# Optimization experiments

Hardware: AMD Instinct MI355X
Metric: run time of the kernel (lower is better)

Reference implementation:

```python
import jax, jax.numpy as jnp
import numpy as np
from jax import lax

GROUPS = 32
EPS = 1e-5
N_STEPS = 8   # fixed-step stand-in for adaptive implicit_adams
N_CORR = 2    # trapezoidal (Adams-Moulton) corrector iterations


def group_norm(x, gamma, beta):
    B, C, H, W = x.shape
    xg = x.reshape(B, GROUPS, C // GROUPS, H, W)
    mean = xg.mean(axis=(2, 3, 4), keepdims=True)
    var = xg.var(axis=(2, 3, 4), keepdims=True)
    xg = (xg - mean) * lax.rsqrt(var + EPS)
    return xg.reshape(B, C, H, W) * gamma[None, :, None, None] + beta[None, :, None, None]


def batch_norm1d(x, gamma, beta):  # training-mode batch stats, x: [B,C,L]
    mean = x.mean(axis=(0, 2), keepdims=True)
    var = x.var(axis=(0, 2), keepdims=True)
    return (x - mean) * lax.rsqrt(var + EPS) * gamma[None, :, None] + beta[None, :, None]


def conv1d(x, w, b):  # x [B,Cin,L], w [Cout,Cin,3], pad=1
    y = lax.conv_general_dilated(x, w, (1,), [(1, 1)], dimension_numbers=('NCH', 'OIH', 'NCH'))
    return y + b[None, :, None]


def concat_conv2d(t, x, w, b):  # x [B,C,H,W], w [C, C+1, 3,3], pad=1
    tt = jnp.full_like(x[:, :1], t)
    ttx = jnp.concatenate([tt, x], axis=1)
    y = lax.conv_general_dilated(ttx, w, (1, 1), [(1, 1), (1, 1)], dimension_numbers=('NCHW', 'OIHW', 'NCHW'))
    return y + b[None, :, None, None]


def make_odefunc(cw1, cb1, gn1_g, gn1_b, gn2_g, gn2_b, cw2, cb2, gn3_g, gn3_b):
    def f(t, x):
        out = jax.nn.relu(group_norm(x, gn1_g, gn1_b))
        out = concat_conv2d(t, out, cw1, cb1)
        out = jax.nn.elu(group_norm(out, gn2_g, gn2_b))
        out = concat_conv2d(t, out, cw2, cb2)
        return group_norm(out, gn3_g, gn3_b)
    return f


def ode_integrate(f, y0):
    h = 1.0 / N_STEPS

    def step(y, i):
        t = i.astype(y.dtype) * h
        f0 = f(t, y)
        y1 = y + h * f0  # explicit predictor
        for _ in range(N_CORR):  # implicit (trapezoidal AM) corrector
            y1 = y + 0.5 * h * (f0 + f(t + h, y1))
        return y1, None

    yT, _ = lax.scan(step, y0, jnp.arange(N_STEPS))
    return yT


def setup_inputs() -> dict:
    key = jax.random.key(0)
    ks = jax.random.split(key, 8)
    B, L, C = 16, 4096, 256
    inp = {
        'x': jax.random.normal(ks[0], (B, 4, 1, L), dtype=jnp.float32),
        'w1': jax.random.normal(ks[1], (64, 4, 3), dtype=jnp.float32) * 0.1,
        'b1': jnp.zeros((64,), jnp.float32),
        'bn1_g': jnp.ones((64,), jnp.float32), 'bn1_b': jnp.zeros((64,), jnp.float32),
        'w2': jax.random.normal(ks[2], (256, 64, 3), dtype=jnp.float32) * 0.05,
        'b2': jnp.zeros((256,), jnp.float32),
        'bn2_g': jnp.ones((256,), jnp.float32), 'bn2_b': jnp.zeros((256,), jnp.float32),
        'cw1': jax.random.normal(ks[3], (C, C + 1, 3, 3), dtype=jnp.float32) * 0.02,
        'cb1': jnp.zeros((C,), jnp.float32),
        'gn1_g': jnp.ones((C,), jnp.float32), 'gn1_b': jnp.zeros((C,), jnp.float32),
        'gn2_g': jnp.ones((C,), jnp.float32), 'gn2_b': jnp.zeros((C,), jnp.float32),
        'cw2': jax.random.normal(ks[4], (C, C + 1, 3, 3), dtype=jnp.float32) * 0.02,
        'cb2': jnp.zeros((C,), jnp.float32),
        'gn3_g': jnp.ones((C,), jnp.float32), 'gn3_b': jnp.zeros((C,), jnp.float32),
    }
    return inp


def reference(x, w1, b1, bn1_g, bn1_b, w2, b2, bn2_g, bn2_b,
              cw1, cb1, gn1_g, gn1_b, gn2_g, gn2_b, cw2, cb2, gn3_g, gn3_b):
    h = x[:, :, 0, :]                       # squeeze(2) -> [B,4,L]
    h = jax.nn.relu(batch_norm1d(conv1d(h, w1, b1), bn1_g, bn1_b))
    h = jnp.tanh(batch_norm1d(conv1d(h, w2, b2), bn2_g, bn2_b))
    y0 = h[:, :, None, :]                   # unsqueeze(2) -> [B,256,1,L]
    f = make_odefunc(cw1, cb1, gn1_g, gn1_b, gn2_g, gn2_b, cw2, cb2, gn3_g, gn3_b)
    return ode_integrate(f, y0)
```

## Files before the change

kernel.cpp:

```cpp
#include <hip/hip_runtime.h>
#include <math.h>

#define L4 4096

typedef short bf16x8 __attribute__((ext_vector_type(8)));
typedef float f32x4 __attribute__((ext_vector_type(4)));

__device__ __forceinline__ unsigned short f2bf(float f) {
  unsigned u = __builtin_bit_cast(unsigned, f);
  return (unsigned short)((u + 0x7FFFu + ((u >> 16) & 1u)) >> 16);
}
__device__ __forceinline__ float bf2f(unsigned short h) {
  unsigned u = ((unsigned)h) << 16;
  return __builtin_bit_cast(float, u);
}
__device__ __forceinline__ unsigned pk2(float lo, float hi) {
  unsigned d;
  asm("v_cvt_pk_bf16_f32 %0, %1, %2" : "=v"(d) : "v"(lo), "v"(hi));
  return d;
}
__device__ __forceinline__ float fast_tanh(float x) {
  float e = __expf(2.f * x);
  return 1.f - 2.f * __builtin_amdgcn_rcpf(e + 1.f);
}

__global__ __launch_bounds__(256) void pack_big(const float* __restrict__ cw,
                                                unsigned short* __restrict__ Apack,
                                                float* __restrict__ Tpack) {
  int gid = blockIdx.x * 256 + threadIdx.x;
  if (gid < 768) {
    int o = gid & 255, tap = gid >> 8;
    Tpack[tap * 256 + o] = cw[((size_t)o * 257) * 9 + 3 + tap];
  }
  if (gid >= 24 * 16 * 64) return;
  int ks = gid >> 10;
  int frow = (gid >> 6) & 15;
  int lane = gid & 63;
  int o = frow * 16 + (lane & 15);
  int tap = ks >> 3;
  int ib = ((ks & 7) << 5) + ((lane >> 4) << 3);
#pragma unroll
  for (int e = 0; e < 8; e++) {
    int i = ib + e;
    Apack[(size_t)gid * 8 + e] = f2bf(cw[((size_t)o * 257 + (i + 1)) * 9 + 3 + tap]);
  }
}

__global__ __launch_bounds__(256) void pack_stem(const float* __restrict__ w2,
                                                 unsigned short* __restrict__ Apack) {
  int gid = blockIdx.x * 256 + threadIdx.x;
  if (gid >= 6 * 16 * 64) return;
  int ks = gid >> 10;
  int frow = (gid >> 6) & 15;
  int lane = gid & 63;
  int o = frow * 16 + (lane & 15);
  int tap = ks >> 1;
  int ib = ((ks & 1) << 5) + ((lane >> 4) << 3);
#pragma unroll
  for (int e = 0; e < 8; e++) {
    int i = ib + e;
    Apack[(size_t)gid * 8 + e] = f2bf(w2[((size_t)o * 64 + i) * 3 + tap]);
  }
}

__global__ __launch_bounds__(256) void conv1_kernel(const float* __restrict__ x,
                                                    const float* __restrict__ w,
                                                    const float* __restrict__ bias,
                                                    unsigned short* __restrict__ out) {
  int idx = blockIdx.x * 256 + threadIdx.x;
  int l = idx & 4095;
  int c = (idx >> 12) & 63;
  int b = idx >> 18;
  const float* xb = x + (size_t)b * 4 * L4;
  const float* wc = w + c * 12;
  float acc = bias[c];
#pragma unroll
  for (int i = 0; i < 4; i++) {
    float x0 = (l > 0) ? xb[i * L4 + l - 1] : 0.f;
    float x1 = xb[i * L4 + l];
    float x2 = (l < 4095) ? xb[i * L4 + l + 1] : 0.f;
    acc += wc[i * 3] * x0 + wc[i * 3 + 1] * x1 + wc[i * 3 + 2] * x2;
  }
  out[idx] = f2bf(acc);
}

__global__ __launch_bounds__(256) void stats_kernel(const float* __restrict__ in,
                                                    float* __restrict__ stats,
                                                    int unit_stride, int nrow,
                                                    int row_stride, int rowlen,
                                                    float inv_n) {
  int u = blockIdx.x;
  const float* base = in + (size_t)u * unit_stride;
  float s = 0.f, s2 = 0.f;
  for (int r = 0; r < nrow; r++) {
    const float* rowp = base + (size_t)r * row_stride;
    for (int j = threadIdx.x * 4; j < rowlen; j += 256 * 4) {
      float4 v = *(const float4*)(rowp + j);
      s += v.x + v.y + v.z + v.w;
      s2 += v.x * v.x + v.y * v.y + v.z * v.z + v.w * v.w;
    }
  }
  __shared__ float sh[512];
  sh[threadIdx.x] = s;
  sh[256 + threadIdx.x] = s2;
  __syncthreads();
  for (int off = 128; off > 0; off >>= 1) {
    if (threadIdx.x < off) {
      sh[threadIdx.x] += sh[threadIdx.x + off];
      sh[256 + threadIdx.x] += sh[256 + threadIdx.x + off];
    }
    __syncthreads();
  }
  if (threadIdx.x == 0) {
    float m = sh[0] * inv_n;
    float var = sh[256] * inv_n - m * m;
    stats[u * 2] = m;
    stats[u * 2 + 1] = rsqrtf(var + 1e-5f);
  }
}

__global__ __launch_bounds__(256) void stats_bf16_kernel(const unsigned short* __restrict__ in,
                                                         float* __restrict__ stats,
                                                         int unit_stride, int nrow,
                                                         int row_stride, int rowlen,
                                                         float inv_n) {
  int u = blockIdx.x;
  const unsigned short* base = in + (size_t)u * unit_stride;
  float s = 0.f, s2 = 0.f;
  for (int r = 0; r < nrow; r++) {
    const unsigned short* rowp = base + (size_t)r * row_stride;
    for (int j = threadIdx.x * 4; j < rowlen; j += 256 * 4) {
      ushort4 v = *(const ushort4*)(rowp + j);
      float va = bf2f(v.x), vb = bf2f(v.y), vc = bf2f(v.z), vd = bf2f(v.w);
      s += va + vb + vc + vd;
      s2 += va * va + vb * vb + vc * vc + vd * vd;
    }
  }
  __shared__ float sh[512];
  sh[threadIdx.x] = s;
  sh[256 + threadIdx.x] = s2;
  __syncthreads();
  for (int off = 128; off > 0; off >>= 1) {
    if (threadIdx.x < off) {
      sh[threadIdx.x] += sh[threadIdx.x + off];
      sh[256 + threadIdx.x] += sh[256 + threadIdx.x + off];
    }
    __syncthreads();
  }
  if (threadIdx.x == 0) {
    float m = sh[0] * inv_n;
    float var = sh[256] * inv_n - m * m;
    stats[u * 2] = m;
    stats[u * 2 + 1] = rsqrtf(var + 1e-5f);
  }
}

__global__ __launch_bounds__(256) void act_transpose64(const unsigned short* __restrict__ inv,
                                                       const float* __restrict__ stats,
                                                       const float* __restrict__ gamma,
                                                       const float* __restrict__ beta,
                                                       unsigned short* __restrict__ Xt) {
  constexpr int C = 64;
  __shared__ unsigned short tile[64 * C];
  int bidx = blockIdx.x;
  int b = bidx >> 6;
  int lt = bidx & 63;
  int l0 = lt << 6;
  int t = threadIdx.x;
  int lanel = t & 63;
  int cq = t >> 6;
  for (int cp = 0; cp < C / 4; cp++) {
    int c = cp * 4 + cq;
    float m = stats[2 * c], rs = stats[2 * c + 1];
    float ga = gamma[c] * rs, be = beta[c] - m * ga;
    size_t gidx = ((size_t)b * C + c) * 4096 + l0 + lanel;
    float v = bf2f(inv[gidx]);
    float a = v * ga + be;
    float r = fmaxf(a, 0.f);
    int sw = (lanel & 15) << 2;
    tile[lanel * C + (c ^ sw)] = f2bf(r);
  }
  __syncthreads();
  constexpr int CH = C / 4;
  constexpr int RPP = 256 / CH;
  for (int p = 0; p < 64 / RPP; p++) {
    int r = p * RPP + t / CH;
    int ch = t % CH;
    int sw = (r & 15) << 2;
    ushort4 v = *(const ushort4*)&tile[r * C + ((ch * 4) ^ sw)];
    *(ushort4*)&Xt[((size_t)b * 4098 + 1 + l0 + r) * C + ch * 4] = v;
  }
  if (lt == 0) {
    if (t < C / 4) *(ushort4*)&Xt[((size_t)b * 4098 + 0) * C + t * 4] = make_ushort4(0, 0, 0, 0);
  } else if (lt == 63) {
    if (t < C / 4) *(ushort4*)&Xt[((size_t)b * 4098 + 4097) * C + t * 4] = make_ushort4(0, 0, 0, 0);
  }
}

template <int NKS, int KLG, int CIN, int NORM, int ACT, int NCH, bool INBF, bool TCH, int OUT>
__global__ __launch_bounds__(512, 4) void gemm_T(const void* __restrict__ Bsrc,
                                                 const unsigned short* __restrict__ Apack,
                                                 const float* __restrict__ Pin,
                                                 const float* __restrict__ gng,
                                                 const float* __restrict__ gnb,
                                                 const float* __restrict__ Tpack,
                                                 const float* __restrict__ bias,
                                                 float tval,
                                                 void* __restrict__ outv,
                                                 float* __restrict__ Pout) {
  constexpr int CPR = CIN / 8;
  constexpr int CPRLG = (CIN == 256) ? 5 : 3;
  constexpr int ROWS = 66;
  constexpr int RPI = 512 >> CPRLG;
  constexpr int TOT = ROWS * CPR;
  __shared__ unsigned short bsm[ROWS * CIN];
  __shared__ float gsm[32][2];
  __shared__ float ebias[256];
  __shared__ float psh[32][2];

  int tid = threadIdx.x;
  int lane = tid & 63;
  int wv = tid >> 6;
  int b = blockIdx.x >> 6;
  int lt = blockIdx.x & 63;
  int l_base = lt << 6;
  int wo0 = wv << 5;
  int col = lane & 15;
  int grp = lane >> 4;

  if (NORM) {
    int g = tid >> 4, j0 = tid & 15;
    const float* Pg = Pin + ((size_t)b * 32 + g) * 128;
    float s = 0.f, s2 = 0.f;
    for (int j = j0; j < NCH; j += 16) { s += Pg[j * 2]; s2 += Pg[j * 2 + 1]; }
#pragma unroll
    for (int off = 8; off; off >>= 1) { s += __shfl_down(s, off, 16); s2 += __shfl_down(s2, off, 16); }
    if (j0 == 0) {
      float m = s * (1.f / 32768.f);
      float var = s2 * (1.f / 32768.f) - m * m;
      gsm[g][0] = m;
      gsm[g][1] = rsqrtf(var + 1e-5f);
    }
  }
  if (tid < 256) {
    float e = bias[tid];
    if (TCH) e += tval * (Tpack[tid] + Tpack[256 + tid] + Tpack[512 + tid]);
    ebias[tid] = e;
  }
  if (OUT == 0 && tid >= 256 && tid < 288) { psh[tid - 256][0] = 0.f; psh[tid - 256][1] = 0.f; }
  __syncthreads();

  {
    int pl = tid & (CPR - 1);
    int row0 = tid >> CPRLG;
    int gch = pl ^ (row0 & 7);
    float ga[8], be[8];
    if (NORM) {
      float m = gsm[gch][0], rs = gsm[gch][1];
      float4 g0 = *(const float4*)&gng[gch * 8];
      float4 g1 = *(const float4*)&gng[gch * 8 + 4];
      float4 b0 = *(const float4*)&gnb[gch * 8];
      float4 b1 = *(const float4*)&gnb[gch * 8 + 4];
      ga[0] = g0.x * rs; ga[1] = g0.y * rs; ga[2] = g0.z * rs; ga[3] = g0.w * rs;
      ga[4] = g1.x * rs; ga[5] = g1.y * rs; ga[6] = g1.z * rs; ga[7] = g1.w * rs;
      be[0] = b0.x - m * ga[0]; be[1] = b0.y - m * ga[1];
      be[2] = b0.z - m * ga[2]; be[3] = b0.w - m * ga[3];
      be[4] = b1.x - m * ga[4]; be[5] = b1.y - m * ga[5];
      be[6] = b1.z - m * ga[6]; be[7] = b1.w - m * ga[7];
    }
#pragma unroll
    for (int it = 0; it < (TOT + 511) / 512; it++) {
      int chunk = it * 512 + tid;
      if (chunk < TOT) {
        int row = row0 + it * RPI;
        uint4 w4;
        if (NORM) {
          int gl = l_base - 1 + row;
          if (gl >= 0 && gl < 4096) {
            size_t base = ((size_t)b * 4096 + gl) * CIN + gch * 8;
            float vv[8];
            if (INBF) {
              bf16x8 raw = *(const bf16x8*)((const unsigned short*)Bsrc + base);
#pragma unroll
              for (int e = 0; e < 8; e++) vv[e] = bf2f((unsigned short)raw[e]);
            } else {
              float4 r0 = *(const float4*)((const float*)Bsrc + base);
              float4 r1 = *(const float4*)((const float*)Bsrc + base + 4);
              vv[0] = r0.x; vv[1] = r0.y; vv[2] = r0.z; vv[3] = r0.w;
              vv[4] = r1.x; vv[5] = r1.y; vv[6] = r1.z; vv[7] = r1.w;
            }
            float rr[8];
#pragma unroll
            for (int e = 0; e < 8; e++) {
              float a = vv[e] * ga[e] + be[e];
              rr[e] = (ACT == 0) ? fmaxf(a, 0.f) : (a > 0.f ? a : __expf(a) - 1.f);
            }
            w4.x = pk2(rr[0], rr[1]); w4.y = pk2(rr[2], rr[3]);
            w4.z = pk2(rr[4], rr[5]); w4.w = pk2(rr[6], rr[7]);
          } else {
            w4 = make_uint4(0, 0, 0, 0);
          }
        } else {
          w4 = *(const uint4*)((const unsigned short*)Bsrc +
                               ((size_t)b * 4098 + l_base + row) * CIN + gch * 8);
        }
        *(uint4*)&bsm[(size_t)chunk * 8] = w4;
      }
    }
  }
  __syncthreads();

  const unsigned short* apk = Apack + (size_t)(wv * 2) * 512 + (size_t)lane * 8;

  f32x4 acc[2][4];
#pragma unroll
  for (int i = 0; i < 2; i++)
#pragma unroll
    for (int j = 0; j < 4; j++) acc[i][j] = (f32x4){0.f, 0.f, 0.f, 0.f};

#pragma unroll
  for (int ks = 0; ks < NKS; ks++) {
    int tap = ks >> KLG;
    int cbase = (ks & ((1 << KLG) - 1)) << 2;
    int lr0 = col + tap;
    int cb = (cbase + grp) ^ (lr0 & 7);
    const unsigned short* bp = &bsm[((size_t)(lr0 << CPRLG) + cb) * 8];
    const unsigned short* ap = apk + (size_t)ks * 16 * 512;
    bf16x8 bfr[4], afr[2];
#pragma unroll
    for (int fc = 0; fc < 4; fc++) bfr[fc] = *(const bf16x8*)(bp + fc * 16 * CIN);
#pragma unroll
    for (int fo = 0; fo < 2; fo++) afr[fo] = *(const bf16x8*)(ap + fo * 512);
#pragma unroll
    for (int fo = 0; fo < 2; fo++)
#pragma unroll
      for (int fc = 0; fc < 4; fc++)
        acc[fo][fc] = __builtin_amdgcn_mfma_f32_16x16x32_bf16(afr[fo], bfr[fc], acc[fo][fc], 0, 0, 0);
  }

  float ps = 0.f, ps2 = 0.f;
#pragma unroll
  for (int fo = 0; fo < 2; fo++) {
    int o0 = wo0 + fo * 16 + grp * 4;
    float eb[4], w0c[4], w2c[4];
#pragma unroll
    for (int r = 0; r < 4; r++) { eb[r] = ebias[o0 + r]; w0c[r] = 0.f; w2c[r] = 0.f; }
    if (TCH && lt == 0) {
#pragma unroll
      for (int r = 0; r < 4; r++) w0c[r] = tval * Tpack[o0 + r];
    }
    if (TCH && lt == 63) {
#pragma unroll
      for (int r = 0; r < 4; r++) w2c[r] = tval * Tpack[512 + o0 + r];
    }
#pragma unroll
    for (int fc = 0; fc < 4; fc++) {
      int l = l_base + fc * 16 + col;
      float v[4];
#pragma unroll
      for (int r = 0; r < 4; r++) {
        v[r] = acc[fo][fc][r] + eb[r];
        if (TCH) {
          if (lt == 0) v[r] -= (l == 0) ? w0c[r] : 0.f;
          if (lt == 63) v[r] -= (l == 4095) ? w2c[r] : 0.f;
        }
        if (OUT == 0) { ps += v[r]; ps2 += v[r] * v[r]; }
      }
      if (OUT == 0) {
        uint2 pk = make_uint2(pk2(v[0], v[1]), pk2(v[2], v[3]));
        *(uint2*)((unsigned short*)outv + ((size_t)b * 4096 + l) * 256 + o0) = pk;
      } else {
#pragma unroll
        for (int r = 0; r < 4; r++)
          ((float*)outv)[((size_t)b * 256 + o0 + r) * 4096 + l] = v[r];
      }
    }
    if (OUT == 0) {
      float s = ps, s2 = ps2;
#pragma unroll
      for (int off = 8; off; off >>= 1) {
        s += __shfl_down(s, off, 16);
        s2 += __shfl_down(s2, off, 16);
      }
      if (col == 0) {
        int g = wv * 4 + fo * 2 + (grp >> 1);
        atomicAdd(&psh[g][0], s);
        atomicAdd(&psh[g][1], s2);
      }
      ps = 0.f; ps2 = 0.f;
    }
  }

  if (OUT == 0) {
    __syncthreads();
    if (tid < 32) {
      size_t pi = ((size_t)b * 32 + tid) * 128 + (size_t)lt * 2;
      Pout[pi] = psh[tid][0];
      Pout[pi + 1] = psh[tid][1];
    }
  }
}

__global__ __launch_bounds__(512) void bn_tanh_T(const float* __restrict__ Q,
                                                 const float* __restrict__ stats,
                                                 const float* __restrict__ gamma,
                                                 const float* __restrict__ beta,
                                                 float* __restrict__ Y,
                                                 float* __restrict__ P1) {
  int tid = threadIdx.x;
  int b = blockIdx.x >> 5;
  int seg = blockIdx.x & 31;
  int c = tid >> 1;
  float m = stats[2 * c], rs = stats[2 * c + 1];
  float ga = gamma[c] * rs, be = beta[c] - m * ga;
  __shared__ float psh[32][2];
  if (tid < 32) { psh[tid][0] = 0.f; psh[tid][1] = 0.f; }
  __syncthreads();
  float s = 0.f, s2 = 0.f;
  for (int it = 0; it < 16; it++) {
    int l4 = (tid & 1) + it * 2;
    int l0 = seg * 128 + l4 * 4;
    float4 v = *(const float4*)&Q[((size_t)b * 256 + c) * 4096 + l0];
    float r0 = fast_tanh(v.x * ga + be);
    float r1 = fast_tanh(v.y * ga + be);
    float r2 = fast_tanh(v.z * ga + be);
    float r3 = fast_tanh(v.w * ga + be);
    Y[((size_t)b * 4096 + l0 + 0) * 256 + c] = r0;
    Y[((size_t)b * 4096 + l0 + 1) * 256 + c] = r1;
    Y[((size_t)b * 4096 + l0 + 2) * 256 + c] = r2;
    Y[((size_t)b * 4096 + l0 + 3) * 256 + c] = r3;
    s += r0 + r1 + r2 + r3;
    s2 += r0 * r0 + r1 * r1 + r2 * r2 + r3 * r3;
  }
#pragma unroll
  for (int off = 8; off; off >>= 1) { s += __shfl_down(s, off, 16); s2 += __shfl_down(s2, off, 16); }
  if ((tid & 15) == 0) {
    int g = c >> 3;
    atomicAdd(&psh[g][0], s);
    atomicAdd(&psh[g][1], s2);
  }
  __syncthreads();
  if (tid < 32) {
    size_t pi = ((size_t)b * 32 + tid) * 128 + (size_t)seg * 2;
    P1[pi] = psh[tid][0];
    P1[pi + 1] = psh[tid][1];
  }
}

template <int MODE>
__global__ __launch_bounds__(512) void combine_T(const unsigned short* __restrict__ F,
                                                 const float* __restrict__ P3,
                                                 const float* __restrict__ gng,
                                                 const float* __restrict__ gnb,
                                                 float* __restrict__ Y,
                                                 unsigned short* __restrict__ Y1,
                                                 float* __restrict__ P1) {
  __shared__ float gsm[32][2];
  __shared__ float gabe[256][2];
  __shared__ float psh[32][2];
  int tid = threadIdx.x;
  int b = blockIdx.x >> 5;
  int seg = blockIdx.x & 31;
  {
    int g = tid >> 4, j0 = tid & 15;
    const float* Pg = P3 + ((size_t)b * 32 + g) * 128;
    float s = 0.f, s2 = 0.f;
    for (int j = j0; j < 64; j += 16) { s += Pg[j * 2]; s2 += Pg[j * 2 + 1]; }
#pragma unroll
    for (int off = 8; off; off >>= 1) { s += __shfl_down(s, off, 16); s2 += __shfl_down(s2, off, 16); }
    if (j0 == 0) {
      float m = s * (1.f / 32768.f);
      float var = s2 * (1.f / 32768.f) - m * m;
      gsm[g][0] = m;
      gsm[g][1] = rsqrtf(var + 1e-5f);
    }
  }
  __syncthreads();
  if (tid < 256) {
    float m = gsm[tid >> 3][0], rs = gsm[tid >> 3][1];
    float ga = gng[tid] * rs;
    gabe[tid][0] = ga;
    gabe[tid][1] = gnb[tid] - m * ga;
  }
  if (tid >= 256 && tid < 288) { psh[tid - 256][0] = 0.f; psh[tid - 256][1] = 0.f; }
  __syncthreads();

  size_t base4 = ((size_t)b * 4096 + seg * 128) * 64;
  int c0 = (tid << 2) & 255;
  int g = c0 >> 3;
  float ga0 = gabe[c0][0], be0 = gabe[c0][1];
  float ga1 = gabe[c0 + 1][0], be1 = gabe[c0 + 1][1];
  float ga2 = gabe[c0 + 2][0], be2 = gabe[c0 + 2][1];
  float ga3 = gabe[c0 + 3][0], be3 = gabe[c0 + 3][1];
  float s = 0.f, s2 = 0.f;
  for (int i = tid; i < 8192; i += 512) {
    size_t idx4 = base4 + i;
    ushort4 fv = ((const ushort4*)F)[idx4];
    float4 yv = ((const float4*)Y)[idx4];
    float f0 = bf2f(fv.x) * ga0 + be0;
    float f1 = bf2f(fv.y) * ga1 + be1;
    float f2 = bf2f(fv.z) * ga2 + be2;
    float f3 = bf2f(fv.w) * ga3 + be3;
    float4 yn;
    yn.x = yv.x + (MODE == 0 ? 0.125f : 0.0625f) * f0;
    yn.y = yv.y + (MODE == 0 ? 0.125f : 0.0625f) * f1;
    yn.z = yv.z + (MODE == 0 ? 0.125f : 0.0625f) * f2;
    yn.w = yv.w + (MODE == 0 ? 0.125f : 0.0625f) * f3;
    if (MODE == 0) {
      float4 yb;
      yb.x = yv.x + 0.0625f * f0;
      yb.y = yv.y + 0.0625f * f1;
      yb.z = yv.z + 0.0625f * f2;
      yb.w = yv.w + 0.0625f * f3;
      ((float4*)Y)[idx4] = yb;
    }
    if (MODE == 2) {
      ((float4*)Y)[idx4] = yn;
    } else {
      uint2 pk = make_uint2(pk2(yn.x, yn.y), pk2(yn.z, yn.w));
      ((uint2*)Y1)[idx4] = pk;
    }
    s += yn.x + yn.y + yn.z + yn.w;
    s2 += yn.x * yn.x + yn.y * yn.y + yn.z * yn.z + yn.w * yn.w;
  }
  s += __shfl_xor(s, 1);
  s2 += __shfl_xor(s2, 1);
  if ((tid & 1) == 0) {
    atomicAdd(&psh[g][0], s);
    atomicAdd(&psh[g][1], s2);
  }
  __syncthreads();
  if (tid < 32) {
    size_t pi = ((size_t)b * 32 + tid) * 128 + (size_t)seg * 2;
    P1[pi] = psh[tid][0];
    P1[pi + 1] = psh[tid][1];
  }
}

__global__ __launch_bounds__(256) void transpose_final(const float* __restrict__ Y,
                                                       float* __restrict__ out) {
  __shared__ float tile[64 * 260];
  int b = blockIdx.x >> 6;
  int lt = blockIdx.x & 63;
  int t = threadIdx.x;
  for (int i = t; i < 4096; i += 256) {
    int r = i >> 6;
    int c4 = (i & 63) << 2;
    float4 v = *(const float4*)&Y[((size_t)b * 4096 + lt * 64 + r) * 256 + c4];
    *(float4*)&tile[r * 260 + c4] = v;
  }
  __syncthreads();
  for (int i = t; i < 4096; i += 256) {
    int c = i >> 4;
    int l4 = (i & 15) << 2;
    float4 v;
    v.x = tile[(l4 + 0) * 260 + c];
    v.y = tile[(l4 + 1) * 260 + c];
    v.z = tile[(l4 + 2) * 260 + c];
    v.w = tile[(l4 + 3) * 260 + c];
    *(float4*)&out[((size_t)b * 256 + c) * 4096 + lt * 64 + l4] = v;
  }
}

extern "C" void kernel_launch(void* const* d_in, const int* in_sizes, int n_in,
                              void* d_out, int out_size, void* d_ws, size_t ws_size,
                              hipStream_t stream) {
  const float* x = (const float*)d_in[0];
  const float* w1 = (const float*)d_in[1];
  const float* b1 = (const float*)d_in[2];
  const float* bn1_g = (const float*)d_in[3];
  const float* bn1_b = (const float*)d_in[4];
  const float* w2 = (const float*)d_in[5];
  const float* b2 = (const float*)d_in[6];
  const float* bn2_g = (const float*)d_in[7];
  const float* bn2_b = (const float*)d_in[8];
  const float* cw1 = (const float*)d_in[9];
  const float* cb1 = (const float*)d_in[10];
  const float* gn1_g = (const float*)d_in[11];
  const float* gn1_b = (const float*)d_in[12];
  const float* gn2_g = (const float*)d_in[13];
  const float* gn2_b = (const float*)d_in[14];
  const float* cw2 = (const float*)d_in[15];
  const float* cb2 = (const float*)d_in[16];
  const float* gn3_g = (const float*)d_in[17];
  const float* gn3_b = (const float*)d_in[18];

  const size_t SZ = (size_t)16 * 256 * 4096;

  char* p = (char*)d_ws;
  float* Ybuf = (float*)p;                   p += SZ * 4;
  unsigned short* C1 = (unsigned short*)p;   p += SZ * 2;
  unsigned short* Fb = (unsigned short*)p;   p += SZ * 2;
  unsigned short* APK1 = (unsigned short*)p; p += (size_t)24 * 16 * 64 * 8 * 2;
  unsigned short* APK2 = (unsigned short*)p; p += (size_t)24 * 16 * 64 * 8 * 2;
  unsigned short* APKS = (unsigned short*)p; p += (size_t)6 * 16 * 64 * 8 * 2;
  float* TP1 = (float*)p;                    p += 768 * 4;
  float* TP2 = (float*)p;                    p += 768 * 4;
  float* STATS = (float*)p;                  p += 1024 * 4;
  float* P1 = (float*)p;                     p += (size_t)16 * 32 * 128 * 4;
  float* P2 = (float*)p;                     p += (size_t)16 * 32 * 128 * 4;
  float* P3 = (float*)p;                     p += (size_t)16 * 32 * 128 * 4;

  float* Q = (float*)d_out;
  unsigned short* Y1 = (unsigned short*)d_out;

  pack_big<<<96, 256, 0, stream>>>(cw1, APK1, TP1);
  pack_big<<<96, 256, 0, stream>>>(cw2, APK2, TP2);
  pack_stem<<<24, 256, 0, stream>>>(w2, APKS);

  conv1_kernel<<<16384, 256, 0, stream>>>(x, w1, b1, C1);
  stats_bf16_kernel<<<64, 256, 0, stream>>>(C1, STATS, 4096, 16, 64 * 4096, 4096, 1.f / 65536.f);
  act_transpose64<<<1024, 256, 0, stream>>>(C1, STATS, bn1_g, bn1_b, Fb);
  gemm_T<6, 1, 64, 0, 0, 32, true, false, 1><<<1024, 512, 0, stream>>>(
      Fb, APKS, nullptr, nullptr, nullptr, nullptr, b2, 0.f, Q, nullptr);
  stats_kernel<<<256, 256, 0, stream>>>(Q, STATS, 4096, 16, 256 * 4096, 4096, 1.f / 65536.f);
  bn_tanh_T<<<512, 512, 0, stream>>>(Q, STATS, bn2_g, bn2_b, Ybuf, P1);

  const float H = 0.125f;
  for (int i = 0; i < 8; i++) {
    float t = i * H;
    gemm_T<24, 3, 256, 1, 0, 32, false, true, 0><<<1024, 512, 0, stream>>>(
        Ybuf, APK1, P1, gn1_g, gn1_b, TP1, cb1, t, C1, P2);
    gemm_T<24, 3, 256, 1, 1, 64, true, true, 0><<<1024, 512, 0, stream>>>(
        C1, APK2, P2, gn2_g, gn2_b, TP2, cb2, t, Fb, P3);
    combine_T<0><<<512, 512, 0, stream>>>(Fb, P3, gn3_g, gn3_b, Ybuf, Y1, P1);
    for (int c = 0; c < 2; c++) {
      gemm_T<24, 3, 256, 1, 0, 32, true, true, 0><<<1024, 512, 0, stream>>>(
          Y1, APK1, P1, gn1_g, gn1_b, TP1, cb1, t + H, C1, P2);
      gemm_T<24, 3, 256, 1, 1, 64, true, true, 0><<<1024, 512, 0, stream>>>(
          C1, APK2, P2, gn2_g, gn2_b, TP2, cb2, t + H, Fb, P3);
      if (c == 0)
        combine_T<1><<<512, 512, 0, stream>>>(Fb, P3, gn3_g, gn3_b, Ybuf, Y1, P1);
      else
        combine_T<2><<<512, 512, 0, stream>>>(Fb, P3, gn3_g, gn3_b, Ybuf, Y1, P1);
    }
  }

  transpose_final<<<1024, 256, 0, stream>>>(Ybuf, (float*)d_out);
}
```

Before: 2.617 ms.

## Process two L-tiles per block, prefetching second tile during first GEMM

Each GEMM block now computes two adjacent 64-column L tiles, with the grid halved. Global loads for the second tile are issued into registers before the first tile's MFMA loop, then normalized and staged into a second LDS buffer. The aim is to hide global-load latency behind matrix math. In exchange, LDS use doubles and register pressure rises, which may lower occupancy, and the grid has half as many blocks.

Measured after the change: 4.332 ms. 65.5% more time.

```diff
diff --git a/kernel.cpp b/kernel.cpp
--- a/kernel.cpp
+++ b/kernel.cpp
@@ -213,7 +213,8 @@
   constexpr int ROWS = 66;
   constexpr int RPI = 512 >> CPRLG;
   constexpr int TOT = ROWS * CPR;
-  __shared__ unsigned short bsm[ROWS * CIN];
+  constexpr int NIT = (TOT + 511) / 512;
+  __shared__ unsigned short bsm[2][ROWS * CIN];
   __shared__ float gsm[32][2];
   __shared__ float ebias[256];
   __shared__ float psh[32][2];
@@ -221,9 +222,10 @@
   int tid = threadIdx.x;
   int lane = tid & 63;
   int wv = tid >> 6;
-  int b = blockIdx.x >> 6;
-  int lt = blockIdx.x & 63;
-  int l_base = lt << 6;
+  int b = blockIdx.x >> 5;
+  int blt = blockIdx.x & 31;
+  int l_base0 = blt << 7;
+  int l_base1 = l_base0 + 64;
   int wo0 = wv << 5;
   int col = lane & 15;
   int grp = lane >> 4;
@@ -250,151 +252,241 @@
   if (OUT == 0 && tid >= 256 && tid < 288) { psh[tid - 256][0] = 0.f; psh[tid - 256][1] = 0.f; }
   __syncthreads();
 
-  {
-    int pl = tid & (CPR - 1);
-    int row0 = tid >> CPRLG;
-    int gch = pl ^ (row0 & 7);
-    float ga[8], be[8];
-    if (NORM) {
-      float m = gsm[gch][0], rs = gsm[gch][1];
-      float4 g0 = *(const float4*)&gng[gch * 8];
-      float4 g1 = *(const float4*)&gng[gch * 8 + 4];
-      float4 b0 = *(const float4*)&gnb[gch * 8];
-      float4 b1 = *(const float4*)&gnb[gch * 8 + 4];
-      ga[0] = g0.x * rs; ga[1] = g0.y * rs; ga[2] = g0.z * rs; ga[3] = g0.w * rs;
-      ga[4] = g1.x * rs; ga[5] = g1.y * rs; ga[6] = g1.z * rs; ga[7] = g1.w * rs;
-      be[0] = b0.x - m * ga[0]; be[1] = b0.y - m * ga[1];
-      be[2] = b0.z - m * ga[2]; be[3] = b0.w - m * ga[3];
-      be[4] = b1.x - m * ga[4]; be[5] = b1.y - m * ga[5];
-      be[6] = b1.z - m * ga[6]; be[7] = b1.w - m * ga[7];
-    }
-#pragma unroll
-    for (int it = 0; it < (TOT + 511) / 512; it++) {
-      int chunk = it * 512 + tid;
-      if (chunk < TOT) {
-        int row = row0 + it * RPI;
-        uint4 w4;
-        if (NORM) {
-          int gl = l_base - 1 + row;
-          if (gl >= 0 && gl < 4096) {
-            size_t base = ((size_t)b * 4096 + gl) * CIN + gch * 8;
-            float vv[8];
-            if (INBF) {
-              bf16x8 raw = *(const bf16x8*)((const unsigned short*)Bsrc + base);
-#pragma unroll
-              for (int e = 0; e < 8; e++) vv[e] = bf2f((unsigned short)raw[e]);
-            } else {
-              float4 r0 = *(const float4*)((const float*)Bsrc + base);
-              float4 r1 = *(const float4*)((const float*)Bsrc + base + 4);
-              vv[0] = r0.x; vv[1] = r0.y; vv[2] = r0.z; vv[3] = r0.w;
-              vv[4] = r1.x; vv[5] = r1.y; vv[6] = r1.z; vv[7] = r1.w;
-            }
-            float rr[8];
-#pragma unroll
-            for (int e = 0; e < 8; e++) {
-              float a = vv[e] * ga[e] + be[e];
-              rr[e] = (ACT == 0) ? fmaxf(a, 0.f) : (a > 0.f ? a : __expf(a) - 1.f);
-            }
-            w4.x = pk2(rr[0], rr[1]); w4.y = pk2(rr[2], rr[3]);
-            w4.z = pk2(rr[4], rr[5]); w4.w = pk2(rr[6], rr[7]);
+  int pl = tid & (CPR - 1);
+  int row0 = tid >> CPRLG;
+  int gch = pl ^ (row0 & 7);
+  float ga[8], be[8];
+  if (NORM) {
+    float m = gsm[gch][0], rs = gsm[gch][1];
+    float4 g0 = *(const float4*)&gng[gch * 8];
+    float4 g1 = *(const float4*)&gng[gch * 8 + 4];
+    float4 b0 = *(const float4*)&gnb[gch * 8];
+    float4 b1 = *(const float4*)&gnb[gch * 8 + 4];
+    ga[0] = g0.x * rs; ga[1] = g0.y * rs; ga[2] = g0.z * rs; ga[3] = g0.w * rs;
+    ga[4] = g1.x * rs; ga[5] = g1.y * rs; ga[6] = g1.z * rs; ga[7] = g1.w * rs;
+    be[0] = b0.x - m * ga[0]; be[1] = b0.y - m * ga[1];
+    be[2] = b0.z - m * ga[2]; be[3] = b0.w - m * ga[3];
+    be[4] = b1.x - m * ga[4]; be[5] = b1.y - m * ga[5];
+    be[6] = b1.z - m * ga[6]; be[7] = b1.w - m * ga[7];
+  }
+
+  auto transform8 = [&](const float* vv) -> uint4 {
+    float rr[8];
+#pragma unroll
+    for (int e = 0; e < 8; e++) {
+      float a = vv[e] * ga[e] + be[e];
+      rr[e] = (ACT == 0) ? fmaxf(a, 0.f) : (a > 0.f ? a : __expf(a) - 1.f);
+    }
+    uint4 w4;
+    w4.x = pk2(rr[0], rr[1]); w4.y = pk2(rr[2], rr[3]);
+    w4.z = pk2(rr[4], rr[5]); w4.w = pk2(rr[6], rr[7]);
+    return w4;
+  };
+
+#pragma unroll
+  for (int it = 0; it < NIT; it++) {
+    int chunk = it * 512 + tid;
+    if (chunk < TOT) {
+      int row = row0 + it * RPI;
+      uint4 w4;
+      if (NORM) {
+        int gl = l_base0 - 1 + row;
+        if (gl >= 0 && gl < 4096) {
+          size_t base = ((size_t)b * 4096 + gl) * CIN + gch * 8;
+          float vv[8];
+          if (INBF) {
+            bf16x8 raw = *(const bf16x8*)((const unsigned short*)Bsrc + base);
+#pragma unroll
+            for (int e = 0; e < 8; e++) vv[e] = bf2f((unsigned short)raw[e]);
           } else {
-            w4 = make_uint4(0, 0, 0, 0);
+            float4 r0 = *(const float4*)((const float*)Bsrc + base);
+            float4 r1 = *(const float4*)((const float*)Bsrc + base + 4);
+            vv[0] = r0.x; vv[1] = r0.y; vv[2] = r0.z; vv[3] = r0.w;
+            vv[4] = r1.x; vv[5] = r1.y; vv[6] = r1.z; vv[7] = r1.w;
           }
+          w4 = transform8(vv);
         } else {
-          w4 = *(const uint4*)((const unsigned short*)Bsrc +
-                               ((size_t)b * 4098 + l_base + row) * CIN + gch * 8);
+          w4 = make_uint4(0, 0, 0, 0);
         }
-        *(uint4*)&bsm[(size_t)chunk * 8] = w4;
+      } else {
+        w4 = *(const uint4*)((const unsigned short*)Bsrc +
+                             ((size_t)b * 4098 + l_base0 + row) * CIN + gch * 8);
       }
-    }
-  }
-  __syncthreads();
+      *(uint4*)&bsm[0][(size_t)chunk * 8] = w4;
+    }
+  }
+  __syncthreads();
+
+  uint4 hA[NIT], hB[NIT];
+#pragma unroll
+  for (int it = 0; it < NIT; it++) {
+    int chunk = it * 512 + tid;
+    if (chunk < TOT) {
+      int row = row0 + it * RPI;
+      if (NORM) {
+        int gl = l_base1 - 1 + row;
+        if (gl >= 0 && gl < 4096) {
+          size_t base = ((size_t)b * 4096 + gl) * CIN + gch * 8;
+          if (INBF) {
+            hA[it] = *(const uint4*)((const unsigned short*)Bsrc + base);
+          } else {
+            hA[it] = *(const uint4*)((const float*)Bsrc + base);
+            hB[it] = *(const uint4*)((const float*)Bsrc + base + 4);
+          }
+        }
+      } else {
+        hA[it] = *(const uint4*)((const unsigned short*)Bsrc +
+                                 ((size_t)b * 4098 + l_base1 + row) * CIN + gch * 8);
+      }
+    }
+  }
 
   const unsigned short* apk = Apack + (size_t)(wv * 2) * 512 + (size_t)lane * 8;
 
   f32x4 acc[2][4];
-#pragma unroll
-  for (int i = 0; i < 2; i++)
-#pragma unroll
-    for (int j = 0; j < 4; j++) acc[i][j] = (f32x4){0.f, 0.f, 0.f, 0.f};
-
-#pragma unroll
-  for (int ks = 0; ks < NKS; ks++) {
-    int tap = ks >> KLG;
-    int cbase = (ks & ((1 << KLG) - 1)) << 2;
-    int lr0 = col + tap;
-    int cb = (cbase + grp) ^ (lr0 & 7);
-    const unsigned short* bp = &bsm[((size_t)(lr0 << CPRLG) + cb) * 8];
-    const unsigned short* ap = apk + (size_t)ks * 16 * 512;
-    bf16x8 bfr[4], afr[2];
-#pragma unroll
-    for (int fc = 0; fc < 4; fc++) bfr[fc] = *(const bf16x8*)(bp + fc * 16 * CIN);
-#pragma unroll
-    for (int fo = 0; fo < 2; fo++) afr[fo] = *(const bf16x8*)(ap + fo * 512);
-#pragma unroll
-    for (int fo = 0; fo < 2; fo++)
-#pragma unroll
-      for (int fc = 0; fc < 4; fc++)
-        acc[fo][fc] = __builtin_amdgcn_mfma_f32_16x16x32_bf16(afr[fo], bfr[fc], acc[fo][fc], 0, 0, 0);
-  }
-
-  float ps = 0.f, ps2 = 0.f;
-#pragma unroll
-  for (int fo = 0; fo < 2; fo++) {
-    int o0 = wo0 + fo * 16 + grp * 4;
-    float eb[4], w0c[4], w2c[4];
-#pragma unroll
-    for (int r = 0; r < 4; r++) { eb[r] = ebias[o0 + r]; w0c[r] = 0.f; w2c[r] = 0.f; }
-    if (TCH && lt == 0) {
-#pragma unroll
-      for (int r = 0; r < 4; r++) w0c[r] = tval * Tpack[o0 + r];
-    }
-    if (TCH && lt == 63) {
-#pragma unroll
-      for (int r = 0; r < 4; r++) w2c[r] = tval * Tpack[512 + o0 + r];
-    }
-#pragma unroll
-    for (int fc = 0; fc < 4; fc++) {
-      int l = l_base + fc * 16 + col;
-      float v[4];
-#pragma unroll
-      for (int r = 0; r < 4; r++) {
-        v[r] = acc[fo][fc][r] + eb[r];
-        if (TCH) {
-          if (lt == 0) v[r] -= (l == 0) ? w0c[r] : 0.f;
-          if (lt == 63) v[r] -= (l == 4095) ? w2c[r] : 0.f;
+  auto zero_acc = [&]() {
+#pragma unroll
+    for (int i = 0; i < 2; i++)
+#pragma unroll
+      for (int j = 0; j < 4; j++) acc[i][j] = (f32x4){0.f, 0.f, 0.f, 0.f};
+  };
+  auto do_mfma = [&](const unsigned short* bsmp) {
+#pragma unroll
+    for (int ks = 0; ks < NKS; ks++) {
+      int tap = ks >> KLG;
+      int cbase = (ks & ((1 << KLG) - 1)) << 2;
+      int lr0 = col + tap;
+      int cb = (cbase + grp) ^ (lr0 & 7);
+      const unsigned short* bp = &bsmp[((size_t)(lr0 << CPRLG) + cb) * 8];
+      const unsigned short* ap = apk + (size_t)ks * 16 * 512;
+      bf16x8 bfr[4], afr[2];
+#pragma unroll
+      for (int fc = 0; fc < 4; fc++) bfr[fc] = *(const bf16x8*)(bp + fc * 16 * CIN);
+#pragma unroll
+      for (int fo = 0; fo < 2; fo++) afr[fo] = *(const bf16x8*)(ap + fo * 512);
+#pragma unroll
+      for (int fo = 0; fo < 2; fo++)
+#pragma unroll
+        for (int fc = 0; fc < 4; fc++)
+          acc[fo][fc] = __builtin_amdgcn_mfma_f32_16x16x32_bf16(afr[fo], bfr[fc], acc[fo][fc], 0, 0, 0);
+    }
+  };
+  auto do_epilogue = [&](int lbase, bool lo, bool hi) {
+    float ps = 0.f, ps2 = 0.f;
+#pragma unroll
+    for (int fo = 0; fo < 2; fo++) {
+      int o0 = wo0 + fo * 16 + grp * 4;
+      float eb[4], w0c[4], w2c[4];
+#pragma unroll
+      for (int r = 0; r < 4; r++) { eb[r] = ebias[o0 + r]; w0c[r] = 0.f; w2c[r] = 0.f; }
+      if (TCH && lo) {
+#pragma unroll
+        for (int r = 0; r < 4; r++) w0c[r] = tval * Tpack[o0 + r];
+      }
+      if (TCH && hi) {
+#pragma unroll
+        for (int r = 0; r < 4; r++) w2c[r] = tval * Tpack[512 + o0 + r];
+      }
+#pragma unroll
+      for (int fc = 0; fc < 4; fc++) {
+        int l = lbase + fc * 16 + col;
+        float v[4];
+#pragma unroll
+        for (int r = 0; r < 4; r++) {
+          v[r] = acc[fo][fc][r] + eb[r];
+          if (TCH) {
+            if (lo) v[r] -= (l == 0) ? w0c[r] : 0.f;
+            if (hi) v[r] -= (l == 4095) ? w2c[r] : 0.f;
+          }
+          if (OUT == 0) { ps += v[r]; ps2 += v[r] * v[r]; }
         }
-        if (OUT == 0) { ps += v[r]; ps2 += v[r] * v[r]; }
+        if (OUT == 0) {
+          uint2 pk = make_uint2(pk2(v[0], v[1]), pk2(v[2], v[3]));
+          *(uint2*)((unsigned short*)outv + ((size_t)b * 4096 + l) * 256 + o0) = pk;
+        } else {
+#pragma unroll
+          for (int r = 0; r < 4; r++)
+            ((float*)outv)[((size_t)b * 256 + o0 + r) * 4096 + l] = v[r];
+        }
       }
       if (OUT == 0) {
-        uint2 pk = make_uint2(pk2(v[0], v[1]), pk2(v[2], v[3]));
-        *(uint2*)((unsigned short*)outv + ((size_t)b * 4096 + l) * 256 + o0) = pk;
+        float s = ps, s2 = ps2;
+#pragma unroll
+        for (int off = 8; off; off >>= 1) {
+          s += __shfl_down(s, off, 16);
+          s2 += __shfl_down(s2, off, 16);
+        }
+        if (col == 0) {
+          int g = wv * 4 + fo * 2 + (grp >> 1);
+          atomicAdd(&psh[g][0], s);
+          atomicAdd(&psh[g][1], s2);
+        }
+        ps = 0.f; ps2 = 0.f;
+      }
+    }
+  };
+
+  zero_acc();
+  do_mfma(bsm[0]);
+  do_epilogue(l_base0, blt == 0, false);
+
+#pragma unroll
+  for (int it = 0; it < NIT; it++) {
+    int chunk = it * 512 + tid;
+    if (chunk < TOT) {
+      int row = row0 + it * RPI;
+      uint4 w4;
+      if (NORM) {
+        int gl = l_base1 - 1 + row;
+        if (gl >= 0 && gl < 4096) {
+          float vv[8];
+          if (INBF) {
+            vv[0] = bf2f((unsigned short)(hA[it].x & 0xFFFF));
+            vv[1] = bf2f((unsigned short)(hA[it].x >> 16));
+            vv[2] = bf2f((unsigned short)(hA[it].y & 0xFFFF));
+            vv[3] = bf2f((unsigned short)(hA[it].y >> 16));
+            vv[4] = bf2f((unsigned short)(hA[it].z & 0xFFFF));
+            vv[5] = bf2f((unsigned short)(hA[it].z >> 16));
+            vv[6] = bf2f((unsigned short)(hA[it].w & 0xFFFF));
+            vv[7] = bf2f((unsigned short)(hA[it].w >> 16));
+          } else {
+            vv[0] = __builtin_bit_cast(float, hA[it].x);
+            vv[1] = __builtin_bit_cast(float, hA[it].y);
+            vv[2] = __builtin_bit_cast(float, hA[it].z);
+            vv[3] = __builtin_bit_cast(float, hA[it].w);
+            vv[4] = __builtin_bit_cast(float, hB[it].x);
+            vv[5] = __builtin_bit_cast(float, hB[it].y);
+            vv[6] = __builtin_bit_cast(float, hB[it].z);
+            vv[7] = __builtin_bit_cast(float, hB[it].w);
+          }
+          w4 = transform8(vv);
+        } else {
+          w4 = make_uint4(0, 0, 0, 0);
+        }
       } else {
-#pragma unroll
-        for (int r = 0; r < 4; r++)
-          ((float*)outv)[((size_t)b * 256 + o0 + r) * 4096 + l] = v[r];
+        w4 = hA[it];
       }
-    }
-    if (OUT == 0) {
-      float s = ps, s2 = ps2;
-#pragma unroll
-      for (int off = 8; off; off >>= 1) {
-        s += __shfl_down(s, off, 16);
-        s2 += __shfl_down(s2, off, 16);
-      }
-      if (col == 0) {
-        int g = wv * 4 + fo * 2 + (grp >> 1);
-        atomicAdd(&psh[g][0], s);
-        atomicAdd(&psh[g][1], s2);
-      }
-      ps = 0.f; ps2 = 0.f;
-    }
-  }
+      *(uint4*)&bsm[1][(size_t)chunk * 8] = w4;
+    }
+  }
+  __syncthreads();
+  if (OUT == 0 && tid < 32) {
+    size_t pi = ((size_t)b * 32 + tid) * 128 + (size_t)(blt * 2) * 2;
+    Pout[pi] = psh[tid][0];
+    Pout[pi + 1] = psh[tid][1];
+    psh[tid][0] = 0.f;
+    psh[tid][1] = 0.f;
+  }
+  __syncthreads();
+
+  zero_acc();
+  do_mfma(bsm[1]);
+  do_epilogue(l_base1, false, blt == 31);
 
   if (OUT == 0) {
     __syncthreads();
     if (tid < 32) {
-      size_t pi = ((size_t)b * 32 + tid) * 128 + (size_t)lt * 2;
+      size_t pi = ((size_t)b * 32 + tid) * 128 + (size_t)(blt * 2 + 1) * 2;
       Pout[pi] = psh[tid][0];
       Pout[pi + 1] = psh[tid][1];
     }
@@ -611,7 +703,7 @@
   conv1_kernel<<<16384, 256, 0, stream>>>(x, w1, b1, C1);
   stats_bf16_kernel<<<64, 256, 0, stream>>>(C1, STATS, 4096, 16, 64 * 4096, 4096, 1.f / 65536.f);
   act_transpose64<<<1024, 256, 0, stream>>>(C1, STATS, bn1_g, bn1_b, Fb);
-  gemm_T<6, 1, 64, 0, 0, 32, true, false, 1><<<1024, 512, 0, stream>>>(
+  gemm_T<6, 1, 64, 0, 0, 32, true, false, 1><<<512, 512, 0, stream>>>(
       Fb, APKS, nullptr, nullptr, nullptr, nullptr, b2, 0.f, Q, nullptr);
   stats_kernel<<<256, 256, 0, stream>>>(Q, STATS, 4096, 16, 256 * 4096, 4096, 1.f / 65536.f);
   bn_tanh_T<<<512, 512, 0, stream>>>(Q, STATS, bn2_g, bn2_b, Ybuf, P1);
@@ -619,15 +711,15 @@
   const float H = 0.125f;
   for (int i = 0; i < 8; i++) {
     float t = i * H;
-    gemm_T<24, 3, 256, 1, 0, 32, false, true, 0><<<1024, 512, 0, stream>>>(
+    gemm_T<24, 3, 256, 1, 0, 32, false, true, 0><<<512, 512, 0, stream>>>(
         Ybuf, APK1, P1, gn1_g, gn1_b, TP1, cb1, t, C1, P2);
-    gemm_T<24, 3, 256, 1, 1, 64, true, true, 0><<<1024, 512, 0, stream>>>(
+    gemm_T<24, 3, 256, 1, 1, 64, true, true, 0><<<512, 512, 0, stream>>>(
         C1, APK2, P2, gn2_g, gn2_b, TP2, cb2, t, Fb, P3);
     combine_T<0><<<512, 512, 0, stream>>>(Fb, P3, gn3_g, gn3_b, Ybuf, Y1, P1);
     for (int c = 0; c < 2; c++) {
-      gemm_T<24, 3, 256, 1, 0, 32, true, true, 0><<<1024, 512, 0, stream>>>(
+      gemm_T<24, 3, 256, 1, 0, 32, true, true, 0><<<512, 512, 0, stream>>>(
           Y1, APK1, P1, gn1_g, gn1_b, TP1, cb1, t + H, C1, P2);
-      gemm_T<24, 3, 256, 1, 1, 64, true, true, 0><<<1024, 512, 0, stream>>>(
+      gemm_T<24, 3, 256, 1, 1, 64, true, true, 0><<<512, 512, 0, stream>>>(
           C1, APK2, P2, gn2_g, gn2_b, TP2, cb2, t + H, Fb, P3);
       if (c == 0)
         combine_T<1><<<512, 512, 0, stream>>>(Fb, P3, gn3_g, gn3_b, Ybuf, Y1, P1);
```
